# Kernel optimization log

Measured on AMD Instinct MI355X. Metric: run time of the kernel, lower is better.

## Reference

```python
import jax, jax.numpy as jnp
import numpy as np

N_NODES = 50000
N_EDGES = 800000
IN_DIM = 128
OUT_DIM = 128
NUM_EDGE_TYPES = 16
RULE_FEAT_DIM = 4


def setup_inputs() -> dict:
    key = jax.random.key(0)
    ks = jax.random.split(key, 20)
    d = OUT_DIM
    s_in = 1.0 / np.sqrt(IN_DIM)
    s_d = 1.0 / np.sqrt(d)
    s_r = 1.0 / np.sqrt(RULE_FEAT_DIM)
    inp = {
        "x": jax.random.normal(ks[0], (N_NODES, IN_DIM), jnp.float32),
        "edge_index": jax.random.randint(ks[1], (2, N_EDGES), 0, N_NODES),
        "edge_type": jax.random.randint(ks[2], (N_EDGES,), 0, NUM_EDGE_TYPES),
        "edge_rule_feat": jax.random.normal(ks[3], (N_EDGES, RULE_FEAT_DIM), jnp.float32),
        "total_nodes": N_NODES,
        # parameters (Linear stored as [in, out]; y = x @ W + b)
        "Wq": jax.random.uniform(ks[4], (IN_DIM, d), jnp.float32, -s_in, s_in),
        "bq": jnp.zeros((d,), jnp.float32),
        "Wk": jax.random.uniform(ks[5], (IN_DIM, d), jnp.float32, -s_in, s_in),
        "bk": jnp.zeros((d,), jnp.float32),
        "Wv": jax.random.uniform(ks[6], (IN_DIM, d), jnp.float32, -s_in, s_in),
        "bv": jnp.zeros((d,), jnp.float32),
        "rel_emb": jax.random.normal(ks[7], (NUM_EDGE_TYPES, d), jnp.float32),
        "attn_vec": jax.random.normal(ks[8], (3 * d,), jnp.float32),
        "rule_w1": jax.random.uniform(ks[9], (RULE_FEAT_DIM, d), jnp.float32, -s_r, s_r),
        "rule_b1": jnp.zeros((d,), jnp.float32),
        "rule_w2": jax.random.uniform(ks[10], (d, 1), jnp.float32, -s_d, s_d),
        "rule_b2": jnp.zeros((1,), jnp.float32),  # zero-initialized in source
        "gate_rule_w": jax.random.uniform(ks[11], (RULE_FEAT_DIM, 1), jnp.float32, -s_r, s_r),
        "gate_rule_b": jnp.zeros((1,), jnp.float32),
        "gate_neural_w": jax.random.uniform(ks[12], (2 * d, 1), jnp.float32, -1.0 / np.sqrt(2 * d), 1.0 / np.sqrt(2 * d)),
        "gate_neural_b": jnp.zeros((1,), jnp.float32),
        "msg_w": jax.random.uniform(ks[13], (d, d), jnp.float32, -s_d, s_d),
        "msg_b": jnp.zeros((d,), jnp.float32),
    }
    return inp


def reference(x, edge_index, edge_type, edge_rule_feat, total_nodes,
              Wq, bq, Wk, bk, Wv, bv, rel_emb, attn_vec,
              rule_w1, rule_b1, rule_w2, rule_b2,
              gate_rule_w, gate_rule_b, gate_neural_w, gate_neural_b,
              msg_w, msg_b):
    src, dst = edge_index[0], edge_index[1]
    d = msg_w.shape[0]

    h_src = x[src] @ Wk + bk                  # [E, d]
    h_dst = x[dst] @ Wq + bq                  # [E, d]
    rel = rel_emb[edge_type]                  # [E, d]

    # (cat([h_src,h_dst,rel]) * attn_vec).sum(-1) without materializing the concat
    a1, a2, a3 = attn_vec[:d], attn_vec[d:2 * d], attn_vec[2 * d:]
    e_base = jax.nn.leaky_relu(h_src @ a1 + h_dst @ a2 + rel @ a3, negative_slope=0.2)

    hidden = jax.nn.relu(edge_rule_feat @ rule_w1 + rule_b1)
    b_ij = (hidden @ rule_w2)[:, 0] + rule_b2[0]          # rule bias per edge

    gate_logit = (edge_rule_feat @ gate_rule_w)[:, 0] + gate_rule_b[0] \
               + (h_src @ gate_neural_w[:d, 0] + h_dst @ gate_neural_w[d:, 0]) + gate_neural_b[0]
    gamma_ij = jax.nn.sigmoid(gate_logit)

    e = e_base + gamma_ij * b_ij

    n = total_nodes
    # segment softmax over dst (numerically stable)
    seg_max = jax.ops.segment_max(e, dst, num_segments=n)
    e_exp = jnp.exp(e - seg_max[dst])
    seg_sum = jax.ops.segment_sum(e_exp, dst, num_segments=n)
    alpha = e_exp / (seg_sum[dst] + 1e-16)

    # eval mode: dropout is identity
    msg = ((x[src] @ Wv + bv + rel) @ msg_w + msg_b) * alpha[:, None]
    out = jax.ops.segment_sum(msg, dst, num_segments=n)   # index_add over dst
    return out, alpha, gamma_ij, b_ij
```

## Files before the change

### kernel.cpp

```cpp
#include <hip/hip_runtime.h>
#include <math.h>


using bf16x8 = __attribute__((ext_vector_type(8))) short;
using f32x4  = __attribute__((ext_vector_type(4))) float;

__device__ __forceinline__ float wave_max(float v) {
    #pragma unroll
    for (int o = 32; o > 0; o >>= 1) v = fmaxf(v, __shfl_xor(v, o, 64));
    return v;
}
__device__ __forceinline__ float wave_sum(float v) {
    #pragma unroll
    for (int o = 32; o > 0; o >>= 1) v += __shfl_xor(v, o, 64);
    return v;
}

__device__ __forceinline__ unsigned bf16rne(float f) {
    unsigned u = __float_as_uint(f);
    return (u + 0x7FFFu + ((u >> 16) & 1u)) >> 16;
}
__device__ __forceinline__ float bflo(unsigned u) { return __uint_as_float(u << 16); }
__device__ __forceinline__ float bfhi(unsigned u) { return __uint_as_float(u & 0xFFFF0000u); }

__global__ void __launch_bounds__(128) precompute_kernel(
    const float* __restrict__ Wq, const float* __restrict__ bq,
    const float* __restrict__ Wk, const float* __restrict__ bk,
    const float* __restrict__ Wv, const float* __restrict__ bv,
    const float* __restrict__ rel_emb, const float* __restrict__ attn_vec,
    const float* __restrict__ msg_w, const float* __restrict__ msg_b,
    const float* __restrict__ gnw, const float* __restrict__ grb,
    const float* __restrict__ gnb,
    const float* __restrict__ rule_w1, const float* __restrict__ rule_b1,
    const float* __restrict__ rule_w2,
    unsigned short* __restrict__ W2bT, float* __restrict__ c2,
    float* __restrict__ wkA, float* __restrict__ wqA,
    float* __restrict__ wkG, float* __restrict__ wqG,
    float* __restrict__ relA, float* __restrict__ relM,
    float* __restrict__ consts,
    float4* __restrict__ w1t, float2* __restrict__ w12)
{
    __shared__ float red[128];
    int bid = blockIdx.x, j = threadIdx.x;

    auto blk_reduce = [&](float v) -> float {
        red[j] = v;
        __syncthreads();
        for (int s = 64; s > 0; s >>= 1) {
            if (j < s) red[j] += red[j + s];
            __syncthreads();
        }
        float r = red[0];
        __syncthreads();
        return r;
    };

    if (bid < 128) {
        int i = bid;
        float acc = 0.f;
        #pragma unroll 8
        for (int k = 0; k < 128; ++k) acc = fmaf(Wv[i * 128 + k], msg_w[k * 128 + j], acc);
        W2bT[j * 128 + i] = (unsigned short)bf16rne(acc);
        float r;
        r = blk_reduce(Wk[i * 128 + j] * attn_vec[j]);        if (j == 0) wkA[i] = r;
        r = blk_reduce(Wq[i * 128 + j] * attn_vec[128 + j]);  if (j == 0) wqA[i] = r;
        r = blk_reduce(Wk[i * 128 + j] * gnw[j]);             if (j == 0) wkG[i] = r;
        r = blk_reduce(Wq[i * 128 + j] * gnw[128 + j]);       if (j == 0) wqG[i] = r;
    } else if (bid < 144) {
        int t = bid - 128;
        float acc = 0.f;
        #pragma unroll 8
        for (int k = 0; k < 128; ++k) acc = fmaf(rel_emb[t * 128 + k], msg_w[k * 128 + j], acc);
        relM[t * 128 + j] = acc;
        float r = blk_reduce(rel_emb[t * 128 + j] * attn_vec[256 + j]);
        if (j == 0) relA[t] = r;
    } else if (bid == 144) {
        float acc = msg_b[j];
        #pragma unroll 8
        for (int k = 0; k < 128; ++k) acc = fmaf(bv[k], msg_w[k * 128 + j], acc);
        c2[j] = acc;
        w1t[j] = make_float4(rule_w1[j], rule_w1[128 + j], rule_w1[256 + j], rule_w1[384 + j]);
        w12[j] = make_float2(rule_b1[j], rule_w2[j]);
    } else {
        float r = blk_reduce(bk[j] * attn_vec[j] + bq[j] * attn_vec[128 + j]);
        if (j == 0) consts[0] = r;
        r = blk_reduce(bk[j] * gnw[j] + bq[j] * gnw[128 + j]);
        if (j == 0) consts[1] = r + grb[0] + gnb[0];
    }
}

__global__ void __launch_bounds__(256) node_kernel(
    const float4* __restrict__ x4, const unsigned short* __restrict__ W2bT,
    const float* __restrict__ c2,
    const float* __restrict__ wkA, const float* __restrict__ wqA,
    const float* __restrict__ wkG, const float* __restrict__ wqG,
    unsigned* __restrict__ Vmb, float2* __restrict__ srcPack,
    float2* __restrict__ dstPack, int* __restrict__ deg, int n_nodes)
{
    __shared__ unsigned short Asu[128][136];
    __shared__ unsigned short Bsu[128][136];
    const int tid = threadIdx.x;
    const int rowBase = blockIdx.x * 128;

    if (tid < 128 && rowBase + tid < n_nodes) deg[rowBase + tid] = 0;

    #pragma unroll
    for (int l = 0; l < 16; ++l) {
        int flat = l * 256 + tid;
        int r = flat >> 5, k4 = flat & 31;
        int row = rowBase + r;
        float4 v = (row < n_nodes) ? x4[row * 32 + k4] : make_float4(0.f, 0.f, 0.f, 0.f);
        uint2 u;
        u.x = bf16rne(v.x) | (bf16rne(v.y) << 16);
        u.y = bf16rne(v.z) | (bf16rne(v.w) << 16);
        *(uint2*)&Asu[r][k4 * 4] = u;
    }
    #pragma unroll
    for (int l = 0; l < 16; ++l) {
        int flat = l * 256 + tid;
        int n = flat >> 5, kq = flat & 31;
        uint2 w = *(const uint2*)&W2bT[n * 128 + kq * 4];
        *(uint2*)&Bsu[n][kq * 4] = w;
    }

    {
        int r = tid & 127, h = tid >> 7;
        int row = rowBase + r;
        if (row < n_nodes) {
            const float4* wa4 = (const float4*)(h ? wqA : wkA);
            const float4* wg4 = (const float4*)(h ? wqG : wkG);
            float sA = 0.f, sG = 0.f;
            #pragma unroll 8
            for (int k4 = 0; k4 < 32; ++k4) {
                float4 xv = x4[row * 32 + k4];
                float4 wa = wa4[k4], wg = wg4[k4];
                sA = fmaf(xv.x, wa.x, fmaf(xv.y, wa.y, fmaf(xv.z, wa.z, fmaf(xv.w, wa.w, sA))));
                sG = fmaf(xv.x, wg.x, fmaf(xv.y, wg.y, fmaf(xv.z, wg.z, fmaf(xv.w, wg.w, sG))));
            }
            if (h) dstPack[row] = make_float2(sA, sG);
            else   srcPack[row] = make_float2(sA, sG);
        }
    }
    __syncthreads();

    const int wave = tid >> 6, lane = tid & 63;
    const int ln = lane & 15, quad = lane >> 4;
    const int wm = (wave & 1) * 64, wn = (wave >> 1) * 64;

    f32x4 acc[4][4];
    #pragma unroll
    for (int i = 0; i < 4; ++i)
        #pragma unroll
        for (int j = 0; j < 4; ++j) acc[i][j] = (f32x4){0.f, 0.f, 0.f, 0.f};

    #pragma unroll
    for (int kc = 0; kc < 4; ++kc) {
        int k0 = kc * 32 + quad * 8;
        bf16x8 afr[4], bfr[4];
        #pragma unroll
        for (int mt = 0; mt < 4; ++mt)
            afr[mt] = *(const bf16x8*)&Asu[wm + mt * 16 + ln][k0];
        #pragma unroll
        for (int nt = 0; nt < 4; ++nt)
            bfr[nt] = *(const bf16x8*)&Bsu[wn + nt * 16 + ln][k0];
        #pragma unroll
        for (int mt = 0; mt < 4; ++mt)
            #pragma unroll
            for (int nt = 0; nt < 4; ++nt)
                acc[mt][nt] = __builtin_amdgcn_mfma_f32_16x16x32_bf16(
                    afr[mt], bfr[nt], acc[mt][nt], 0, 0, 0);
    }

    #pragma unroll
    for (int nt = 0; nt < 4; ++nt) {
        int col = wn + nt * 16 + ln;
        float cb = c2[col];
        #pragma unroll
        for (int mt = 0; mt < 4; ++mt) {
            #pragma unroll
            for (int r = 0; r < 4; ++r) {
                int row = rowBase + wm + mt * 16 + quad * 4 + r;
                float v = acc[mt][nt][r] + cb;
                float pv = __shfl_xor(v, 1, 64);
                if (!(ln & 1) && row < n_nodes) {
                    Vmb[row * 64 + (col >> 1)] = bf16rne(v) | (bf16rne(pv) << 16);
                }
            }
        }
    }
}

__global__ void __launch_bounds__(256) edge1_kernel(
    const int* __restrict__ ei, const int* __restrict__ et,
    const float4* __restrict__ erf,
    const float4* __restrict__ w1t, const float2* __restrict__ w12,
    const float* __restrict__ rule_b2, const float* __restrict__ grw,
    const float2* __restrict__ srcPack, const float2* __restrict__ dstPack,
    const float* __restrict__ relA, const float* __restrict__ consts,
    float* __restrict__ e_val, float* __restrict__ gamma_out,
    float* __restrict__ b_out, int* __restrict__ deg,
    int n_edges)
{
    int e = blockIdx.x * 256 + threadIdx.x;
    if (e >= n_edges) return;

    int s = ei[e], d = ei[n_edges + e], t = et[e];
    float4 rf = erf[e];
    float2 ss = srcPack[s], dd = dstPack[d];

    float pre = ss.x + dd.x + relA[t] + consts[0];
    float e_base = pre >= 0.f ? pre : 0.2f * pre;

    float b0 = 0.f, b1 = 0.f, b2a = 0.f, b3 = 0.f;
    #pragma unroll 2
    for (int j = 0; j < 128; j += 4) {
        float4 wA = w1t[j + 0], wB = w1t[j + 1], wC = w1t[j + 2], wD = w1t[j + 3];
        float2 cA = w12[j + 0], cB = w12[j + 1], cC = w12[j + 2], cD = w12[j + 3];
        float hA = fmaf(rf.x, wA.x, fmaf(rf.y, wA.y, fmaf(rf.z, wA.z, fmaf(rf.w, wA.w, cA.x))));
        float hB = fmaf(rf.x, wB.x, fmaf(rf.y, wB.y, fmaf(rf.z, wB.z, fmaf(rf.w, wB.w, cB.x))));
        float hC = fmaf(rf.x, wC.x, fmaf(rf.y, wC.y, fmaf(rf.z, wC.z, fmaf(rf.w, wC.w, cC.x))));
        float hD = fmaf(rf.x, wD.x, fmaf(rf.y, wD.y, fmaf(rf.z, wD.z, fmaf(rf.w, wD.w, cD.x))));
        b0  = fmaf(fmaxf(hA, 0.f), cA.y, b0);
        b1  = fmaf(fmaxf(hB, 0.f), cB.y, b1);
        b2a = fmaf(fmaxf(hC, 0.f), cC.y, b2a);
        b3  = fmaf(fmaxf(hD, 0.f), cD.y, b3);
    }
    float b = (b0 + b1) + (b2a + b3) + rule_b2[0];

    float gl = fmaf(rf.x, grw[0], fmaf(rf.y, grw[1],
               fmaf(rf.z, grw[2], fmaf(rf.w, grw[3], consts[1] + ss.y + dd.y))));
    float gamma = 1.f / (1.f + __expf(-gl));

    gamma_out[e] = gamma;
    b_out[e] = b;
    e_val[e] = e_base + gamma * b;
    atomicAdd(&deg[d], 1);
}

__global__ void __launch_bounds__(256) scan1_kernel(
    const int* __restrict__ deg, int* __restrict__ rowPtr,
    int* __restrict__ partials, int n)
{
    __shared__ int sdata[256];
    int tid = threadIdx.x;
    int base = blockIdx.x * 1024 + tid * 4;
    int v0 = (base + 0 < n) ? deg[base + 0] : 0;
    int v1 = (base + 1 < n) ? deg[base + 1] : 0;
    int v2 = (base + 2 < n) ? deg[base + 2] : 0;
    int v3 = (base + 3 < n) ? deg[base + 3] : 0;
    int tsum = v0 + v1 + v2 + v3;
    sdata[tid] = tsum;
    __syncthreads();
    #pragma unroll
    for (int off = 1; off < 256; off <<= 1) {
        int t = (tid >= off) ? sdata[tid - off] : 0;
        __syncthreads();
        sdata[tid] += t;
        __syncthreads();
    }
    int excl = sdata[tid] - tsum;
    if (base + 0 < n) rowPtr[base + 0] = excl;
    if (base + 1 < n) rowPtr[base + 1] = excl + v0;
    if (base + 2 < n) rowPtr[base + 2] = excl + v0 + v1;
    if (base + 3 < n) rowPtr[base + 3] = excl + v0 + v1 + v2;
    if (tid == 255) partials[blockIdx.x] = sdata[255];
}

__global__ void __launch_bounds__(64) scan2_kernel(int* __restrict__ partials, int nb)
{
    int lane = threadIdx.x;
    int v = (lane < nb) ? partials[lane] : 0;
    int orig = v;
    #pragma unroll
    for (int off = 1; off < 64; off <<= 1) {
        int t = __shfl_up(v, off, 64);
        if (lane >= off) v += t;
    }
    if (lane < nb) partials[lane] = v - orig;
}

__global__ void __launch_bounds__(256) scan3_kernel(
    int* __restrict__ rowPtr, const int* __restrict__ partials,
    int* __restrict__ bucketCursor, int n, int n_edges)
{
    int off = partials[blockIdx.x];
    int base = blockIdx.x * 1024 + threadIdx.x * 4;
    #pragma unroll
    for (int k = 0; k < 4; ++k) {
        int idx = base + k;
        if (idx < n) {
            int r = rowPtr[idx] + off;
            rowPtr[idx] = r;
            if ((idx & 255) == 0) bucketCursor[idx >> 8] = r;
        }
    }
    if (blockIdx.x == 0 && threadIdx.x == 0) rowPtr[n] = n_edges;
}

__global__ void __launch_bounds__(256) sort1_kernel(
    const int* __restrict__ ei, const int* __restrict__ et,
    const float* __restrict__ e_val, int* __restrict__ bucketCursor,
    float2* __restrict__ tmp, int n_edges)
{
    __shared__ float2 data[4096];
    __shared__ unsigned char slotB[4096];
    __shared__ int cnt[256], rk[256], base_[256], run[256], scanBuf[256];
    const int tid = threadIdx.x;
    const int blockBase = blockIdx.x * 4096;
    const int total = min(4096, n_edges - blockBase);

    cnt[tid] = 0;
    rk[tid] = 0;
    __syncthreads();

    int   d_[16];
    float ev_[16];
    int   pk_[16];
    #pragma unroll
    for (int i = 0; i < 16; ++i) {
        int e = blockBase + i * 256 + tid;
        if (e < n_edges) {
            int d = ei[n_edges + e];
            d_[i]  = d;
            ev_[i] = e_val[e];
            pk_[i] = (ei[e] & 0xFFFF) | ((et[e] & 15) << 16) | ((d & 255) << 20);
            atomicAdd(&cnt[d >> 8], 1);
        } else {
            d_[i] = -1;
        }
    }
    __syncthreads();

    int c = cnt[tid];
    scanBuf[tid] = c;
    __syncthreads();
    #pragma unroll
    for (int off = 1; off < 256; off <<= 1) {
        int t = (tid >= off) ? scanBuf[tid - off] : 0;
        __syncthreads();
        scanBuf[tid] += t;
        __syncthreads();
    }
    base_[tid] = scanBuf[tid] - c;
    run[tid] = c ? atomicAdd(&bucketCursor[tid], c) : 0;
    __syncthreads();

    #pragma unroll
    for (int i = 0; i < 16; ++i) {
        if (d_[i] >= 0) {
            int b = d_[i] >> 8;
            int r = atomicAdd(&rk[b], 1);
            int slot = base_[b] + r;
            data[slot] = make_float2(ev_[i], __int_as_float(pk_[i]));
            slotB[slot] = (unsigned char)b;
        }
    }
    __syncthreads();

    for (int j = tid; j < total; j += 256) {
        int b = slotB[j];
        tmp[run[b] + (j - base_[b])] = data[j];
    }
}

__global__ void __launch_bounds__(256) sort2_kernel(
    const int* __restrict__ rowPtr, const float2* __restrict__ tmp,
    float2* __restrict__ payload, int n_nodes)
{
    __shared__ int cur[256];
    const int tid = threadIdx.x;
    const int d0 = blockIdx.x * 256;
    const int dEnd = min(d0 + 256, n_nodes);
    if (d0 + tid < dEnd) cur[tid] = rowPtr[d0 + tid];
    __syncthreads();
    const int lo = rowPtr[d0];
    const int hi = rowPtr[dEnd];
    for (int j = lo + tid; j < hi; j += 256) {
        float2 p = tmp[j];
        unsigned pk = __float_as_uint(p.y);
        int dl = (pk >> 20) & 255;
        int pos = atomicAdd(&cur[dl], 1);
        unsigned st = (pk & 0xFFFFu) | (((pk >> 16) & 15u) << 27);
        payload[pos] = make_float2(p.x, __uint_as_float(st));
    }
}

__global__ void __launch_bounds__(256) gather_kernel(
    const int* __restrict__ rowPtr, const float2* __restrict__ payload,
    const unsigned* __restrict__ Vmb, const float* __restrict__ relM,
    float* __restrict__ out, float2* __restrict__ nodeMS, int n_nodes)
{
    __shared__ float2 s_relM[16 * 64];
    const int tid = threadIdx.x;
    const float2* relM2 = (const float2*)relM;
    #pragma unroll
    for (int i = 0; i < 4; ++i) s_relM[i * 256 + tid] = relM2[i * 256 + tid];
    __syncthreads();

    int lane = tid & 63;
    int d = blockIdx.x * 4 + (tid >> 6);
    if (d >= n_nodes) return;
    int start = rowPtr[d];
    int deg = rowPtr[d + 1] - start;

    float acc0 = 0.f, acc1 = 0.f;
    float m = -INFINITY, inv;

    auto acc8 = [&](float av, int st, int k) {
        float a[8];
        int s[8];
        #pragma unroll
        for (int i = 0; i < 8; ++i) {
            a[i] = __shfl(av, k + i, 64);
            s[i] = __shfl(st, k + i, 64);
        }
        unsigned v[8];
        float2 rm[8];
        #pragma unroll
        for (int i = 0; i < 8; ++i) {
            int ss = s[i] & 0x7FFFFFF;
            int tt = ((unsigned)s[i]) >> 27;
            v[i]  = Vmb[ss * 64 + lane];
            rm[i] = s_relM[tt * 64 + lane];
        }
        #pragma unroll
        for (int i = 0; i < 8; ++i) {
            acc0 = fmaf(a[i], bflo(v[i]) + rm[i].x, acc0);
            acc1 = fmaf(a[i], bfhi(v[i]) + rm[i].y, acc1);
        }
    };

    if (deg <= 64) {
        float ev = -INFINITY;
        int st = 0;
        if (lane < deg) {
            float2 p = payload[start + lane];
            ev = p.x;
            st = __float_as_int(p.y);
        }
        m = wave_max(ev);
        float ex = (lane < deg) ? __expf(ev - m) : 0.f;
        float sum = wave_sum(ex);
        inv = 1.f / (sum + 1e-16f);
        float av = ex * inv;
        for (int k = 0; k < deg; k += 8) acc8(av, st, k);
    } else {
        for (int i = lane; i < deg; i += 64) m = fmaxf(m, payload[start + i].x);
        m = wave_max(m);
        float sum = 0.f;
        for (int i = lane; i < deg; i += 64) sum += __expf(payload[start + i].x - m);
        sum = wave_sum(sum);
        inv = 1.f / (sum + 1e-16f);
        for (int c = 0; c < deg; c += 64) {
            int i = c + lane;
            float av = 0.f;
            int st = 0;
            if (i < deg) {
                float2 p = payload[start + i];
                av = __expf(p.x - m) * inv;
                st = __float_as_int(p.y);
            }
            int cnt = min(64, deg - c);
            for (int k = 0; k < cnt; k += 8) acc8(av, st, k);
        }
    }
    if (lane == 0) nodeMS[d] = make_float2(m, inv);
    *(float2*)&out[d * 128 + lane * 2] = make_float2(acc0, acc1);
}

__global__ void __launch_bounds__(256) alpha_kernel(
    const int* __restrict__ ei, const float* __restrict__ e_val,
    const float2* __restrict__ nodeMS, float* __restrict__ alpha_out, int n_edges)
{
    int e = blockIdx.x * blockDim.x + threadIdx.x;
    if (e >= n_edges) return;
    int d = ei[n_edges + e];
    float2 ms = nodeMS[d];
    alpha_out[e] = __expf(e_val[e] - ms.x) * ms.y;
}

extern "C" void kernel_launch(void* const* d_in, const int* in_sizes, int n_in,
                              void* d_out, int out_size, void* d_ws, size_t ws_size,
                              hipStream_t stream)
{
    const float* x        = (const float*)d_in[0];
    const int*   ei       = (const int*)d_in[1];
    const int*   et       = (const int*)d_in[2];
    const float* erf      = (const float*)d_in[3];
    const float* Wq       = (const float*)d_in[5];
    const float* bq       = (const float*)d_in[6];
    const float* Wk       = (const float*)d_in[7];
    const float* bk       = (const float*)d_in[8];
    const float* Wv       = (const float*)d_in[9];
    const float* bv       = (const float*)d_in[10];
    const float* rel_emb  = (const float*)d_in[11];
    const float* attn_vec = (const float*)d_in[12];
    const float* rule_w1  = (const float*)d_in[13];
    const float* rule_b1  = (const float*)d_in[14];
    const float* rule_w2  = (const float*)d_in[15];
    const float* rule_b2  = (const float*)d_in[16];
    const float* grw      = (const float*)d_in[17];
    const float* grb      = (const float*)d_in[18];
    const float* gnw      = (const float*)d_in[19];
    const float* gnb      = (const float*)d_in[20];
    const float* msg_w    = (const float*)d_in[21];
    const float* msg_b    = (const float*)d_in[22];

    const int n_nodes = in_sizes[0] / 128;
    const int n_edges = in_sizes[2];
    const int nb = (n_nodes + 1023) / 1024;
    const int nbuck = (n_nodes + 255) / 256;

    float* ws = (float*)d_ws;
    size_t off = 0;
    unsigned* Vmb  = (unsigned*)(ws + off); off += (size_t)n_nodes * 64;
    float2* payload = (float2*)(ws + off); off += 2 * (size_t)n_edges;
    float2* tmpPay  = (float2*)(ws + off); off += 2 * (size_t)n_edges;
    float* e_val   = ws + off; off += n_edges;
    float* srcPack = ws + off; off += 2 * (size_t)n_nodes;
    float* dstPack = ws + off; off += 2 * (size_t)n_nodes;
    float2* nodeMS = (float2*)(ws + off); off += 2 * (size_t)n_nodes;
    int*   deg     = (int*)(ws + off); off += n_nodes;
    int*   rowPtr  = (int*)(ws + off); off += n_nodes + 4;
    int*   partials= (int*)(ws + off); off += 64;
    int*   bucketCursor = (int*)(ws + off); off += 256;
    unsigned short* W2bT = (unsigned short*)(ws + off); off += 128 * 64;
    float* c2      = ws + off; off += 128;
    float* wkA     = ws + off; off += 128;
    float* wqA     = ws + off; off += 128;
    float* wkG     = ws + off; off += 128;
    float* wqG     = ws + off; off += 128;
    float* relA    = ws + off; off += 16;
    float* relM    = ws + off; off += 16 * 128;
    float* consts  = ws + off; off += 2;
    off += 2;
    float4* w1t    = (float4*)(ws + off); off += 128 * 4;
    float2* w12    = (float2*)(ws + off); off += 128 * 2;

    float* out       = (float*)d_out;
    float* alpha_out = out + (size_t)n_nodes * 128;
    float* gamma_out = alpha_out + n_edges;
    float* b_out     = gamma_out + n_edges;

    hipLaunchKernelGGL(precompute_kernel, dim3(146), dim3(128), 0, stream,
                       Wq, bq, Wk, bk, Wv, bv, rel_emb, attn_vec, msg_w, msg_b,
                       gnw, grb, gnb, rule_w1, rule_b1, rule_w2,
                       W2bT, c2, wkA, wqA, wkG, wqG, relA, relM, consts, w1t, w12);

    hipLaunchKernelGGL(node_kernel, dim3((n_nodes + 127) / 128), dim3(256), 0, stream,
                       (const float4*)x, W2bT, c2,
                       wkA, wqA, wkG, wqG, Vmb, (float2*)srcPack, (float2*)dstPack,
                       deg, n_nodes);

    hipLaunchKernelGGL(edge1_kernel, dim3((n_edges + 255) / 256), dim3(256), 0, stream,
                       ei, et, (const float4*)erf, (const float4*)w1t, (const float2*)w12,
                       rule_b2, grw, (const float2*)srcPack, (const float2*)dstPack,
                       relA, consts, e_val, gamma_out, b_out, deg, n_edges);

    hipLaunchKernelGGL(scan1_kernel, dim3(nb), dim3(256), 0, stream,
                       deg, rowPtr, partials, n_nodes);
    hipLaunchKernelGGL(scan2_kernel, dim3(1), dim3(64), 0, stream,
                       partials, nb);
    hipLaunchKernelGGL(scan3_kernel, dim3(nb), dim3(256), 0, stream,
                       rowPtr, partials, bucketCursor, n_nodes, n_edges);

    hipLaunchKernelGGL(sort1_kernel, dim3((n_edges + 4095) / 4096), dim3(256), 0, stream,
                       ei, et, e_val, bucketCursor, tmpPay, n_edges);

    hipLaunchKernelGGL(sort2_kernel, dim3(nbuck), dim3(256), 0, stream,
                       rowPtr, tmpPay, payload, n_nodes);

    hipLaunchKernelGGL(gather_kernel, dim3((n_nodes + 3) / 4), dim3(256), 0, stream,
                       rowPtr, payload, Vmb, relM, out, nodeMS, n_nodes);

    hipLaunchKernelGGL(alpha_kernel, dim3((n_edges + 255) / 256), dim3(256), 0, stream,
                       ei, e_val, nodeMS, alpha_out, n_edges);
}
```

Before: 279.5 us.

## Compute per-edge rule MLP with split-bf16 MFMA instead of scalar FMAs

The edge1 kernel's rule-bias MLP (4->128 ReLU ->1) is moved from per-thread scalar FMA loops onto 16x16x32 bf16 MFMA instructions. Inputs and weights are split into high and low bf16 parts so the products keep near-fp32 accuracy. Partial sums are reduced across lanes with shuffles and passed to the per-edge threads through shared memory. This cuts the VALU work in edge1 but adds a block barrier and shared-memory traffic, and accuracy now depends on the split-bf16 products.

```diff
diff --git a/kernel.cpp b/kernel.cpp
--- a/kernel.cpp
+++ b/kernel.cpp
@@ -22,6 +22,12 @@
 }
 __device__ __forceinline__ float bflo(unsigned u) { return __uint_as_float(u << 16); }
 __device__ __forceinline__ float bfhi(unsigned u) { return __uint_as_float(u & 0xFFFF0000u); }
+
+__device__ __forceinline__ void splitbf(float x, unsigned& h, unsigned& l) {
+    h = bf16rne(x);
+    float fh = __uint_as_float(h << 16);
+    l = bf16rne(x - fh);
+}
 
 __global__ void __launch_bounds__(128) precompute_kernel(
     const float* __restrict__ Wq, const float* __restrict__ bq,
@@ -201,34 +207,78 @@
     float* __restrict__ b_out, int* __restrict__ deg,
     int n_edges)
 {
-    int e = blockIdx.x * 256 + threadIdx.x;
+    __shared__ float Lb[4][64];
+    const int tid = threadIdx.x;
+    const int wave = tid >> 6, lane = tid & 63;
+    const int ln = lane & 15, quad = lane >> 4;
+    const int e0 = blockIdx.x * 256 + wave * 64;
+    const bf16x8 zf = (bf16x8)(short)0;
+
+    bf16x8 bfr[8];
+    float b1v[8], w2v[8];
+    #pragma unroll
+    for (int nt = 0; nt < 8; ++nt) {
+        int j = nt * 16 + ln;
+        float4 w = w1t[j];
+        float2 c = w12[j];
+        b1v[nt] = c.x;
+        w2v[nt] = c.y;
+        unsigned h0, h1, h2, h3, l0, l1, l2, l3;
+        splitbf(w.x, h0, l0); splitbf(w.y, h1, l1);
+        splitbf(w.z, h2, l2); splitbf(w.w, h3, l3);
+        bf16x8 fh, fl;
+        fh[0] = (short)h0; fh[1] = (short)h1; fh[2] = (short)h2; fh[3] = (short)h3;
+        fh[4] = (short)h0; fh[5] = (short)h1; fh[6] = (short)h2; fh[7] = (short)h3;
+        fl[0] = (short)l0; fl[1] = (short)l1; fl[2] = (short)l2; fl[3] = (short)l3;
+        fl[4] = (short)l0; fl[5] = (short)l1; fl[6] = (short)l2; fl[7] = (short)l3;
+        bfr[nt] = (quad == 0) ? fh : ((quad == 1) ? fl : zf);
+    }
+
+    #pragma unroll
+    for (int mt = 0; mt < 4; ++mt) {
+        int em = e0 + mt * 16 + ln;
+        float4 rf = erf[min(em, n_edges - 1)];
+        unsigned h0, h1, h2, h3, l0, l1, l2, l3;
+        splitbf(rf.x, h0, l0); splitbf(rf.y, h1, l1);
+        splitbf(rf.z, h2, l2); splitbf(rf.w, h3, l3);
+        bf16x8 a;
+        a[0] = (short)h0; a[1] = (short)h1; a[2] = (short)h2; a[3] = (short)h3;
+        a[4] = (short)l0; a[5] = (short)l1; a[6] = (short)l2; a[7] = (short)l3;
+        a = (quad < 2) ? a : zf;
+
+        f32x4 ap = (f32x4){0.f, 0.f, 0.f, 0.f};
+        #pragma unroll
+        for (int nt = 0; nt < 8; ++nt) {
+            f32x4 dd = __builtin_amdgcn_mfma_f32_16x16x32_bf16(
+                a, bfr[nt], (f32x4){0.f, 0.f, 0.f, 0.f}, 0, 0, 0);
+            #pragma unroll
+            for (int r = 0; r < 4; ++r)
+                ap[r] = fmaf(fmaxf(dd[r] + b1v[nt], 0.f), w2v[nt], ap[r]);
+        }
+        #pragma unroll
+        for (int o = 1; o <= 8; o <<= 1) {
+            #pragma unroll
+            for (int r = 0; r < 4; ++r) ap[r] += __shfl_xor(ap[r], o, 64);
+        }
+        if (ln == 0)
+            *(float4*)&Lb[wave][mt * 16 + quad * 4] =
+                make_float4(ap[0], ap[1], ap[2], ap[3]);
+    }
+    __syncthreads();
+
+    int e = e0 + lane;
     if (e >= n_edges) return;
+    float b = Lb[wave][lane] + rule_b2[0];
 
     int s = ei[e], d = ei[n_edges + e], t = et[e];
     float4 rf = erf[e];
-    float2 ss = srcPack[s], dd = dstPack[d];
-
-    float pre = ss.x + dd.x + relA[t] + consts[0];
+    float2 ss = srcPack[s], dd2 = dstPack[d];
+
+    float pre = ss.x + dd2.x + relA[t] + consts[0];
     float e_base = pre >= 0.f ? pre : 0.2f * pre;
 
-    float b0 = 0.f, b1 = 0.f, b2a = 0.f, b3 = 0.f;
-    #pragma unroll 2
-    for (int j = 0; j < 128; j += 4) {
-        float4 wA = w1t[j + 0], wB = w1t[j + 1], wC = w1t[j + 2], wD = w1t[j + 3];
-        float2 cA = w12[j + 0], cB = w12[j + 1], cC = w12[j + 2], cD = w12[j + 3];
-        float hA = fmaf(rf.x, wA.x, fmaf(rf.y, wA.y, fmaf(rf.z, wA.z, fmaf(rf.w, wA.w, cA.x))));
-        float hB = fmaf(rf.x, wB.x, fmaf(rf.y, wB.y, fmaf(rf.z, wB.z, fmaf(rf.w, wB.w, cB.x))));
-        float hC = fmaf(rf.x, wC.x, fmaf(rf.y, wC.y, fmaf(rf.z, wC.z, fmaf(rf.w, wC.w, cC.x))));
-        float hD = fmaf(rf.x, wD.x, fmaf(rf.y, wD.y, fmaf(rf.z, wD.z, fmaf(rf.w, wD.w, cD.x))));
-        b0  = fmaf(fmaxf(hA, 0.f), cA.y, b0);
-        b1  = fmaf(fmaxf(hB, 0.f), cB.y, b1);
-        b2a = fmaf(fmaxf(hC, 0.f), cC.y, b2a);
-        b3  = fmaf(fmaxf(hD, 0.f), cD.y, b3);
-    }
-    float b = (b0 + b1) + (b2a + b3) + rule_b2[0];
-
     float gl = fmaf(rf.x, grw[0], fmaf(rf.y, grw[1],
-               fmaf(rf.z, grw[2], fmaf(rf.w, grw[3], consts[1] + ss.y + dd.y))));
+               fmaf(rf.z, grw[2], fmaf(rf.w, grw[3], consts[1] + ss.y + dd2.y))));
     float gamma = 1.f / (1.f + __expf(-gl));
 
     gamma_out[e] = gamma;
```

Result: slower. 289.4 us (+3.5%).

## Split rule-bias MLP into separate shared-memory tiled kernel processing four edges per thread

Applied to the files above, without the earlier changes.

The per-edge rule MLP (4->128->1) moves out of the gather-heavy edge kernel into its own kernel. That kernel stages the weights in LDS and has each thread compute four edges, so each weight load is reused across four edges. The remaining edge kernel reads the precomputed bias from global memory. The aim is to cut redundant weight loads and separate compute-bound work from latency-bound gathers, at the cost of an extra launch and an extra global write and read of the bias array.

```diff
diff --git a/kernel.cpp b/kernel.cpp
--- a/kernel.cpp
+++ b/kernel.cpp
@@ -190,49 +190,72 @@
     }
 }
 
-__global__ void __launch_bounds__(256) edge1_kernel(
-    const int* __restrict__ ei, const int* __restrict__ et,
+__global__ void __launch_bounds__(256) edge1a_kernel(
     const float4* __restrict__ erf,
     const float4* __restrict__ w1t, const float2* __restrict__ w12,
-    const float* __restrict__ rule_b2, const float* __restrict__ grw,
+    const float* __restrict__ rule_b2,
+    float* __restrict__ b_out, int n_edges)
+{
+    __shared__ float4 s_w1t[128];
+    __shared__ float2 s_w12[128];
+    const int tid = threadIdx.x;
+    if (tid < 128) { s_w1t[tid] = w1t[tid]; s_w12[tid] = w12[tid]; }
+    __syncthreads();
+
+    const int eb = blockIdx.x * 1024;
+    float4 rf[4];
+    #pragma unroll
+    for (int q = 0; q < 4; ++q) {
+        int e = eb + q * 256 + tid;
+        rf[q] = erf[min(e, n_edges - 1)];
+    }
+
+    float bacc[4] = {0.f, 0.f, 0.f, 0.f};
+    #pragma unroll 2
+    for (int j = 0; j < 128; ++j) {
+        float4 w = s_w1t[j];
+        float2 c = s_w12[j];
+        #pragma unroll
+        for (int q = 0; q < 4; ++q) {
+            float h = fmaf(rf[q].x, w.x, fmaf(rf[q].y, w.y,
+                      fmaf(rf[q].z, w.z, fmaf(rf[q].w, w.w, c.x))));
+            bacc[q] = fmaf(fmaxf(h, 0.f), c.y, bacc[q]);
+        }
+    }
+
+    const float rb2 = rule_b2[0];
+    #pragma unroll
+    for (int q = 0; q < 4; ++q) {
+        int e = eb + q * 256 + tid;
+        if (e < n_edges) b_out[e] = bacc[q] + rb2;
+    }
+}
+
+__global__ void __launch_bounds__(256) edge1b_kernel(
+    const int* __restrict__ ei, const int* __restrict__ et,
+    const float4* __restrict__ erf, const float* __restrict__ grw,
     const float2* __restrict__ srcPack, const float2* __restrict__ dstPack,
     const float* __restrict__ relA, const float* __restrict__ consts,
+    const float* __restrict__ b_out,
     float* __restrict__ e_val, float* __restrict__ gamma_out,
-    float* __restrict__ b_out, int* __restrict__ deg,
-    int n_edges)
+    int* __restrict__ deg, int n_edges)
 {
     int e = blockIdx.x * 256 + threadIdx.x;
     if (e >= n_edges) return;
 
     int s = ei[e], d = ei[n_edges + e], t = et[e];
     float4 rf = erf[e];
+    float b = b_out[e];
     float2 ss = srcPack[s], dd = dstPack[d];
 
     float pre = ss.x + dd.x + relA[t] + consts[0];
     float e_base = pre >= 0.f ? pre : 0.2f * pre;
-
-    float b0 = 0.f, b1 = 0.f, b2a = 0.f, b3 = 0.f;
-    #pragma unroll 2
-    for (int j = 0; j < 128; j += 4) {
-        float4 wA = w1t[j + 0], wB = w1t[j + 1], wC = w1t[j + 2], wD = w1t[j + 3];
-        float2 cA = w12[j + 0], cB = w12[j + 1], cC = w12[j + 2], cD = w12[j + 3];
-        float hA = fmaf(rf.x, wA.x, fmaf(rf.y, wA.y, fmaf(rf.z, wA.z, fmaf(rf.w, wA.w, cA.x))));
-        float hB = fmaf(rf.x, wB.x, fmaf(rf.y, wB.y, fmaf(rf.z, wB.z, fmaf(rf.w, wB.w, cB.x))));
-        float hC = fmaf(rf.x, wC.x, fmaf(rf.y, wC.y, fmaf(rf.z, wC.z, fmaf(rf.w, wC.w, cC.x))));
-        float hD = fmaf(rf.x, wD.x, fmaf(rf.y, wD.y, fmaf(rf.z, wD.z, fmaf(rf.w, wD.w, cD.x))));
-        b0  = fmaf(fmaxf(hA, 0.f), cA.y, b0);
-        b1  = fmaf(fmaxf(hB, 0.f), cB.y, b1);
-        b2a = fmaf(fmaxf(hC, 0.f), cC.y, b2a);
-        b3  = fmaf(fmaxf(hD, 0.f), cD.y, b3);
-    }
-    float b = (b0 + b1) + (b2a + b3) + rule_b2[0];
 
     float gl = fmaf(rf.x, grw[0], fmaf(rf.y, grw[1],
                fmaf(rf.z, grw[2], fmaf(rf.w, grw[3], consts[1] + ss.y + dd.y))));
     float gamma = 1.f / (1.f + __expf(-gl));
 
     gamma_out[e] = gamma;
-    b_out[e] = b;
     e_val[e] = e_base + gamma * b;
     atomicAdd(&deg[d], 1);
 }
@@ -552,10 +575,14 @@
                        wkA, wqA, wkG, wqG, Vmb, (float2*)srcPack, (float2*)dstPack,
                        deg, n_nodes);
 
-    hipLaunchKernelGGL(edge1_kernel, dim3((n_edges + 255) / 256), dim3(256), 0, stream,
-                       ei, et, (const float4*)erf, (const float4*)w1t, (const float2*)w12,
-                       rule_b2, grw, (const float2*)srcPack, (const float2*)dstPack,
-                       relA, consts, e_val, gamma_out, b_out, deg, n_edges);
+    hipLaunchKernelGGL(edge1a_kernel, dim3((n_edges + 1023) / 1024), dim3(256), 0, stream,
+                       (const float4*)erf, (const float4*)w1t, (const float2*)w12,
+                       rule_b2, b_out, n_edges);
+
+    hipLaunchKernelGGL(edge1b_kernel, dim3((n_edges + 255) / 256), dim3(256), 0, stream,
+                       ei, et, (const float4*)erf, grw,
+                       (const float2*)srcPack, (const float2*)dstPack,
+                       relA, consts, b_out, e_val, gamma_out, deg, n_edges);
 
     hipLaunchKernelGGL(scan1_kernel, dim3(nb), dim3(256), 0, stream,
                        deg, rowPtr, partials, n_nodes);
```

Result: slower. 296.4 us (+6.1%).
